# Optimization experiments

Hardware: AMD Instinct MI355X
Metric: run time of the kernel (lower is better)

## Reference

```python
import jax, jax.numpy as jnp
import numpy as np

B, C, H, W = 8, 128, 64, 64
GROUPS = 8
EPS = 1e-5


def setup_inputs() -> dict:
    key = jax.random.key(0)
    ks = jax.random.split(key, 4)
    x = jax.random.normal(ks[0], (B, C, H, W), dtype=jnp.float32)
    gamma = jnp.ones((C,), jnp.float32)
    beta = jnp.zeros((C,), jnp.float32)
    w_qkv = jax.random.normal(ks[1], (3 * C, C), jnp.float32) * (C ** -0.5)
    b_qkv = jnp.zeros((3 * C,), jnp.float32)
    w_proj = jax.random.normal(ks[2], (C, C), jnp.float32) * (C ** -0.5)
    b_proj = jnp.zeros((C,), jnp.float32)
    return {"x": x, "gamma": gamma, "beta": beta, "w_qkv": w_qkv,
            "b_qkv": b_qkv, "w_proj": w_proj, "b_proj": b_proj}


def group_norm(x, gamma, beta):
    b, c, h, w = x.shape
    xg = x.reshape(b, GROUPS, c // GROUPS, h, w)
    mean = xg.mean(axis=(2, 3, 4), keepdims=True)
    var = xg.var(axis=(2, 3, 4), keepdims=True)
    xn = ((xg - mean) * jax.lax.rsqrt(var + EPS)).reshape(b, c, h, w)
    return xn * gamma[None, :, None, None] + beta[None, :, None, None]


def reference(x, gamma, beta, w_qkv, b_qkv, w_proj, b_proj):
    b, c, h, w = x.shape
    n = h * w
    hn = group_norm(x, gamma, beta)
    # 1x1 conv == channel matmul
    qkv = jnp.einsum('oc,bchw->bohw', w_qkv, hn) + b_qkv[None, :, None, None]
    q, k, v = jnp.split(qkv.reshape(b, 3 * c, n), 3, axis=1)  # each [b,c,n]
    attn = jax.nn.softmax(jnp.einsum('bci,bcj->bij', q, k) * (c ** -0.5), axis=-1)
    out = jnp.einsum('bij,bcj->bci', attn, v).reshape(b, c, h, w)
    proj = jnp.einsum('oc,bchw->bohw', w_proj, out) + b_proj[None, :, None, None]
    return x + proj
```

## Files before the change

### kernel.cpp

```cpp
#include <hip/hip_runtime.h>
#include <cstdint>

#define NB 8
#define NC 128
#define NPIX 4096
#define NGROUP 8
#define CPG 16
#define EPS_GN 1e-5f
#define QSCALE 0.12751879523604132f
#define NSPLIT 2
#define JTILES (NPIX / 64 / NSPLIT)

typedef __attribute__((ext_vector_type(8))) short short8;
typedef __attribute__((ext_vector_type(16))) float f32x16;

typedef __attribute__((address_space(1))) const void gvoid_t;
typedef __attribute__((address_space(3))) void svoid_t;

__device__ __forceinline__ unsigned packbf(float lo, float hi) {
  unsigned r;
  asm("v_cvt_pk_bf16_f32 %0, %1, %2" : "=v"(r) : "v"(lo), "v"(hi));
  return r;
}
__device__ __forceinline__ ushort bf16of(float v) {
  return (ushort)(packbf(v, v) & 0xffffu);
}
__device__ __forceinline__ float bfl(unsigned w) {
  return __builtin_bit_cast(float, w << 16);
}
__device__ __forceinline__ float bfh(unsigned w) {
  return __builtin_bit_cast(float, w & 0xffff0000u);
}

__device__ __forceinline__ int swK(int row) {
  return ((row & 7) << 1) | ((row >> 3) & 1);
}

__global__ __launch_bounds__(256) void k_wprep(const float* __restrict__ wqkv,
                                               const float* __restrict__ wproj,
                                               ushort* __restrict__ wbuf) {
  int gi = blockIdx.x * 256 + threadIdx.x;
  int t = gi >> 11, ci = gi & 2047;
  int o = ci >> 4, cc = (ci & 15) ^ (o & 7);
  const float* src = (t < 3) ? (wqkv + ((size_t)(t * 128 + o) * 128 + cc * 8))
                             : (wproj + ((size_t)o * 128 + cc * 8));
  float4 a = *(const float4*)src;
  float4 b2 = *(const float4*)(src + 4);
  uint4 pk;
  pk.x = packbf(a.x, a.y);  pk.y = packbf(a.z, a.w);
  pk.z = packbf(b2.x, b2.y); pk.w = packbf(b2.z, b2.w);
  *(uint4*)&wbuf[(size_t)gi << 3] = pk;
}

__global__ __launch_bounds__(256) void k_gn_stats(const float* __restrict__ x,
                                                  float* __restrict__ stats) {
  int blk = blockIdx.x;
  const float4* base = (const float4*)(x + (size_t)blk * CPG * NPIX);
  float s = 0.f, ss = 0.f;
  for (int i = threadIdx.x; i < CPG * NPIX / 4; i += 256) {
    float4 v = base[i];
    s  += v.x + v.y + v.z + v.w;
    ss += v.x * v.x + v.y * v.y + v.z * v.z + v.w * v.w;
  }
#pragma unroll
  for (int off = 32; off >= 1; off >>= 1) {
    s  += __shfl_down(s, off);
    ss += __shfl_down(ss, off);
  }
  __shared__ float red[8];
  int wid = threadIdx.x >> 6;
  if ((threadIdx.x & 63) == 0) { red[wid] = s; red[4 + wid] = ss; }
  __syncthreads();
  if (threadIdx.x == 0) {
    float S  = red[0] + red[1] + red[2] + red[3];
    float SS = red[4] + red[5] + red[6] + red[7];
    float mean = S * (1.f / (CPG * NPIX));
    float var  = SS * (1.f / (CPG * NPIX)) - mean * mean;
    stats[blk * 2]     = mean;
    stats[blk * 2 + 1] = rsqrtf(var + EPS_GN);
  }
}

__global__ __launch_bounds__(256) void k_qkv(const float* __restrict__ x,
                                             const float* __restrict__ stats,
                                             const float* __restrict__ gamma,
                                             const float* __restrict__ beta,
                                             const ushort* __restrict__ wbuf,
                                             const float* __restrict__ bias,
                                             ushort* __restrict__ qT,
                                             ushort* __restrict__ kT,
                                             ushort* __restrict__ vB) {
  __shared__ ushort At[128 * 128];
  __shared__ ushort Bt[128 * 128];
  __shared__ float sArr[128], tArr[128], biasS[384];
  int b = blockIdx.x, pt = blockIdx.y;
  int p0 = pt * 128;
  int tid = threadIdx.x;
  if (tid < 128) {
    int g = tid >> 4;
    float mean = stats[(b * NGROUP + g) * 2];
    float rstd = stats[(b * NGROUP + g) * 2 + 1];
    float sc = rstd * gamma[tid];
    sArr[tid] = sc;
    tArr[tid] = beta[tid] - mean * sc;
  }
  for (int i = tid; i < 384; i += 256) biasS[i] = bias[i];
  __syncthreads();
  const float* xb = x + (size_t)b * NC * NPIX;
#pragma unroll
  for (int u = 0; u < 8; ++u) {
    int task = tid + u * 256;
    int p = task & 127, cc = task >> 7;
    int c0 = cc * 8;
    float v[8];
#pragma unroll
    for (int i = 0; i < 8; ++i)
      v[i] = sArr[c0 + i] * xb[(size_t)(c0 + i) * NPIX + p0 + p] + tArr[c0 + i];
    uint4 pk;
    pk.x = packbf(v[0], v[1]); pk.y = packbf(v[2], v[3]);
    pk.z = packbf(v[4], v[5]); pk.w = packbf(v[6], v[7]);
    *(uint4*)&Bt[((p << 4) + (cc ^ (p & 7))) << 3] = pk;
  }
  int lane = tid & 63, wv = tid >> 6;
  int lq = lane & 31, h = lane >> 5;

  for (int ot = 0; ot < 3; ++ot) {
    __syncthreads();
#pragma unroll
    for (int u = 0; u < 8; ++u) {
      int g = u * 4 + wv;
      __builtin_amdgcn_global_load_lds(
          (gvoid_t*)(wbuf + (((size_t)ot * 2048 + g * 64 + lane) << 3)),
          (svoid_t*)(At + (g << 9)), 16, 0, 0);
    }
    __syncthreads();
    short8 af[8];
    int arow = wv * 32 + lq;
#pragma unroll
    for (int kk = 0; kk < 8; ++kk) {
      int ch = kk * 2 + h;
      af[kk] = *(const short8*)&At[((arow << 4) + (ch ^ (arow & 7))) << 3];
    }
#pragma unroll
    for (int np = 0; np < 2; ++np) {
      int nt0 = np * 2, nt1 = np * 2 + 1;
      int br0 = nt0 * 32 + lq, br1 = nt1 * 32 + lq;
      f32x16 a0, a1;
#pragma unroll
      for (int r = 0; r < 16; ++r) { a0[r] = 0.f; a1[r] = 0.f; }
      __builtin_amdgcn_s_setprio(1);
#pragma unroll
      for (int kk = 0; kk < 8; ++kk) {
        int ch = kk * 2 + h;
        short8 h0 = *(const short8*)&Bt[((br0 << 4) + (ch ^ (br0 & 7))) << 3];
        short8 h1 = *(const short8*)&Bt[((br1 << 4) + (ch ^ (br1 & 7))) << 3];
        a0 = __builtin_amdgcn_mfma_f32_32x32x16_bf16(af[kk], h0, a0, 0, 0, 0);
        a1 = __builtin_amdgcn_mfma_f32_32x32x16_bf16(af[kk], h1, a1, 0, 0, 0);
      }
      __builtin_amdgcn_s_setprio(0);
#pragma unroll
      for (int half = 0; half < 2; ++half) {
        f32x16& acc = half ? a1 : a0;
        int pg = p0 + (half ? nt1 : nt0) * 32 + lq;
        if (ot < 2) {
          ushort* dst = (ot == 0) ? qT : kT;
          float sc = (ot == 0) ? QSCALE : 1.0f;
#pragma unroll
          for (int g2 = 0; g2 < 4; ++g2) {
            int orow = wv * 32 + 4 * h + 8 * g2;
            uint2 st;
            st.x = packbf((acc[g2 * 4 + 0] + biasS[ot * 128 + orow + 0]) * sc,
                          (acc[g2 * 4 + 1] + biasS[ot * 128 + orow + 1]) * sc);
            st.y = packbf((acc[g2 * 4 + 2] + biasS[ot * 128 + orow + 2]) * sc,
                          (acc[g2 * 4 + 3] + biasS[ot * 128 + orow + 3]) * sc);
            *(uint2*)&dst[(((size_t)b << 12) + pg) * 128 + orow] = st;
          }
        } else {
#pragma unroll
          for (int r = 0; r < 16; ++r) {
            int orow = wv * 32 + (r & 3) + 8 * (r >> 2) + 4 * h;
            float vv = acc[r] + biasS[256 + orow];
            vB[((size_t)(b * 128 + orow) << 12) + pg] = bf16of(vv);
          }
        }
      }
    }
  }
}

__device__ __forceinline__ void attn_tile(const ushort* __restrict__ cur,
                                          const short8 (&qf)[8],
                                          f32x16 (&pacc)[4],
                                          float& m_run, float& l_run,
                                          int lq, int h, int swk) {
  f32x16 s0, s1;
#pragma unroll
  for (int r = 0; r < 16; ++r) { s0[r] = 0.f; s1[r] = 0.f; }
  __builtin_amdgcn_s_setprio(1);
#pragma unroll
  for (int kk = 0; kk < 8; ++kk) {
    int ch = (kk << 1) + h;
    short8 kf0 = *(const short8*)&cur[(((lq) << 4) + (ch ^ swk)) << 3];
    short8 kf1 = *(const short8*)&cur[(((32 + lq) << 4) + (ch ^ swk)) << 3];
    s0 = __builtin_amdgcn_mfma_f32_32x32x16_bf16(kf0, qf[kk], s0, 0, 0, 0);
    s1 = __builtin_amdgcn_mfma_f32_32x32x16_bf16(kf1, qf[kk], s1, 0, 0, 0);
  }
  __builtin_amdgcn_s_setprio(0);

  float tm[8];
#pragma unroll
  for (int r = 0; r < 8; ++r)
    tm[r] = fmaxf(fmaxf(s0[2 * r], s0[2 * r + 1]), fmaxf(s1[2 * r], s1[2 * r + 1]));
  float tmax = fmaxf(fmaxf(fmaxf(tm[0], tm[1]), fmaxf(tm[2], tm[3])),
                     fmaxf(fmaxf(tm[4], tm[5]), fmaxf(tm[6], tm[7])));
  tmax = fmaxf(tmax, __shfl_xor(tmax, 32));

  bool noresc = __all(tmax - m_run <= 8.f);
  float mcur = noresc ? m_run : fmaxf(m_run, tmax);

#pragma unroll
  for (int r = 0; r < 16; ++r) { s0[r] = exp2f(s0[r] - mcur); }
#pragma unroll
  for (int r = 0; r < 16; ++r) { s1[r] = exp2f(s1[r] - mcur); }
  float a0 = (s0[0] + s0[1]) + (s0[2] + s0[3]);
  float a1 = (s0[4] + s0[5]) + (s0[6] + s0[7]);
  float a2 = (s0[8] + s0[9]) + (s0[10] + s0[11]);
  float a3 = (s0[12] + s0[13]) + (s0[14] + s0[15]);
  float a4 = (s1[0] + s1[1]) + (s1[2] + s1[3]);
  float a5 = (s1[4] + s1[5]) + (s1[6] + s1[7]);
  float a6 = (s1[8] + s1[9]) + (s1[10] + s1[11]);
  float a7 = (s1[12] + s1[13]) + (s1[14] + s1[15]);
  float sum = ((a0 + a1) + (a2 + a3)) + ((a4 + a5) + (a6 + a7));
  sum += __shfl_xor(sum, 32);

  if (noresc) {
    l_run += sum;
  } else {
    float alpha = exp2f(m_run - mcur);
    m_run = mcur;
    l_run = l_run * alpha + sum;
#pragma unroll
    for (int r = 0; r < 16; ++r) {
      int qr = (r & 3) + ((r >> 2) << 3) + (h << 2);
      float av = __shfl(alpha, qr);
      pacc[0][r] *= av; pacc[1][r] *= av; pacc[2][r] *= av; pacc[3][r] *= av;
    }
  }

  short8 pa[4];
#pragma unroll
  for (int kk = 0; kk < 4; ++kk) {
    float v0, v1, v2, v3, v4, v5, v6, v7;
    if (kk == 0)      { v0=s0[0];v1=s0[1];v2=s0[2];v3=s0[3];v4=s0[4];v5=s0[5];v6=s0[6];v7=s0[7]; }
    else if (kk == 1) { v0=s0[8];v1=s0[9];v2=s0[10];v3=s0[11];v4=s0[12];v5=s0[13];v6=s0[14];v7=s0[15]; }
    else if (kk == 2) { v0=s1[0];v1=s1[1];v2=s1[2];v3=s1[3];v4=s1[4];v5=s1[5];v6=s1[6];v7=s1[7]; }
    else              { v0=s1[8];v1=s1[9];v2=s1[10];v3=s1[11];v4=s1[12];v5=s1[13];v6=s1[14];v7=s1[15]; }
    unsigned P0a = packbf(v0, v1), P0b = packbf(v2, v3);
    unsigned P1a = packbf(v4, v5), P1b = packbf(v6, v7);
    unsigned sA = h ? P0a : P1a, sB = h ? P0b : P1b;
    unsigned rA = (unsigned)__shfl_xor((int)sA, 32);
    unsigned rB = (unsigned)__shfl_xor((int)sB, 32);
    uint4 wv;
    wv.x = h ? rA : P0a;  wv.y = h ? rB : P0b;
    wv.z = h ? P1a : rA;  wv.w = h ? P1b : rB;
    pa[kk] = __builtin_bit_cast(short8, wv);
  }

  __builtin_amdgcn_s_setprio(1);
#pragma unroll
  for (int nt = 0; nt < 4; ++nt) {
    int row = (nt << 5) + lq;
#pragma unroll
    for (int kk = 0; kk < 4; ++kk) {
      int ch = (kk << 1) + h;
      short8 vf = *(const short8*)&cur[8192 + (((row << 3) + (ch ^ (lq & 7))) << 3)];
      pacc[nt] = __builtin_amdgcn_mfma_f32_32x32x16_bf16(pa[kk], vf, pacc[nt], 0, 0, 0);
    }
  }
  __builtin_amdgcn_s_setprio(0);
}

__global__ __launch_bounds__(256, 2) void k_attn(const ushort* __restrict__ qT,
                                                 const ushort* __restrict__ kT,
                                                 const ushort* __restrict__ vB,
                                                 ushort* __restrict__ attP,
                                                 float2* __restrict__ mlv) {
  __shared__ ushort lds[32768];
  int tid = threadIdx.x;
  int b = blockIdx.x, qt = blockIdx.y, s = blockIdx.z;
  int wid = tid >> 6;
  int lane = tid & 63;
  int lq = lane & 31;
  int h = lane >> 5;
  int swk = swK(lq);
  int q0 = qt * 128 + wid * 32;
  int jbase = s * (NPIX / NSPLIT);

  short8 qf[8];
  const ushort* qp = qT + (((size_t)b << 12) + q0 + lq) * 128 + h * 8;
#pragma unroll
  for (int kk = 0; kk < 8; ++kk) qf[kk] = *(const short8*)(qp + kk * 16);

  f32x16 pacc[4];
#pragma unroll
  for (int nt = 0; nt < 4; ++nt)
#pragma unroll
    for (int r = 0; r < 16; ++r) pacc[nt][r] = 0.f;
  float m_run = -1e30f, l_run = 0.f;

  int id0 = wid * 64 + lane;
  int krow0 = id0 >> 4, kch0 = id0 & 15;
  int vrow0 = id0 >> 3, vch0 = id0 & 7;
  const ushort* kbase = kT + (((size_t)b << 12) + jbase + krow0) * 128 +
                        ((kch0 ^ swK(krow0)) << 3);
  const ushort* vbase = vB + ((size_t)(b * 128 + vrow0) << 12) + jbase +
                        ((vch0 ^ (vrow0 & 7)) << 3);
  int tstage = 0;

#define STAGE(SEL)                                                              \
  do {                                                                          \
    if (tstage < JTILES) {                                                      \
      ushort* dbase = lds + (SEL) * 16384;                                      \
      _Pragma("unroll") for (int u = 0; u < 4; ++u) {                           \
        __builtin_amdgcn_global_load_lds((gvoid_t*)(kbase + u * 2048),          \
            (svoid_t*)(dbase + (u * 4 + wid) * 512), 16, 0, 0);                 \
        __builtin_amdgcn_global_load_lds((gvoid_t*)(vbase + u * 131072),        \
            (svoid_t*)(dbase + 8192 + (u * 4 + wid) * 512), 16, 0, 0);          \
      }                                                                         \
      kbase += 8192;                                       \
      vbase += 64;                                                 \
      ++tstage;                                                                 \
    }                                                                           \
  } while (0)

  STAGE(0);
  for (int it = 0; it < JTILES / 2; ++it) {
    __syncthreads();
    STAGE(1);
    attn_tile(lds, qf, pacc, m_run, l_run, lq, h, swk);
    __syncthreads();
    STAGE(0);
    attn_tile(lds + 16384, qf, pacc, m_run, l_run, lq, h, swk);
  }
#undef STAGE

  size_t sb = (size_t)(s * NB + b);
#pragma unroll
  for (int r = 0; r < 16; ++r) {
    int qr = (r & 3) + ((r >> 2) << 3) + (h << 2);
    size_t rowbase = (((sb << 12) + q0 + qr) << 7) + lq;
    attP[rowbase]      = bf16of(pacc[0][r]);
    attP[rowbase + 32] = bf16of(pacc[1][r]);
    attP[rowbase + 64] = bf16of(pacc[2][r]);
    attP[rowbase + 96] = bf16of(pacc[3][r]);
  }
  if (h == 0) {
    mlv[(sb << 12) + q0 + lq] = make_float2(m_run, l_run);
  }
}

__global__ __launch_bounds__(256) void k_proj(const float* __restrict__ x,
                                              const ushort* __restrict__ attP,
                                              const float2* __restrict__ mlv,
                                              const ushort* __restrict__ wbuf,
                                              const float* __restrict__ bias,
                                              float* __restrict__ out) {
  __shared__ ushort At[128 * 128];
  __shared__ ushort Bt[128 * 128];
  __shared__ float c0s[128], c1s[128], biasS[128];
  int b = blockIdx.x, pt = blockIdx.y;
  int p0 = pt * 128;
  int tid = threadIdx.x;
  int lane = tid & 63, wv = tid >> 6;
#pragma unroll
  for (int u = 0; u < 8; ++u) {
    int g = u * 4 + wv;
    __builtin_amdgcn_global_load_lds(
        (gvoid_t*)(wbuf + (((size_t)3 * 2048 + g * 64 + lane) << 3)),
        (svoid_t*)(At + (g << 9)), 16, 0, 0);
  }
  if (tid < 128) {
    float2 ml0 = mlv[(((size_t)b) << 12) + p0 + tid];
    float2 ml1 = mlv[(((size_t)(NB + b)) << 12) + p0 + tid];
    float M = fmaxf(ml0.x, ml1.x);
    float e0 = exp2f(ml0.x - M), e1 = exp2f(ml1.x - M);
    float inv = 1.f / (ml0.y * e0 + ml1.y * e1);
    c0s[tid] = e0 * inv;
    c1s[tid] = e1 * inv;
    biasS[tid] = bias[tid];
  }
  __syncthreads();
#pragma unroll
  for (int u = 0; u < 8; ++u) {
    int task = tid + u * 256;
    int p = task & 127, cc = task >> 7;
    const ushort* a0p = attP + ((((size_t)b << 12) + p0 + p) << 7) + cc * 8;
    const ushort* a1p = attP + ((((size_t)(NB + b) << 12) + p0 + p) << 7) + cc * 8;
    uint4 u0 = *(const uint4*)a0p;
    uint4 u1 = *(const uint4*)a1p;
    float c0 = c0s[p], c1 = c1s[p];
    uint4 pk;
    pk.x = packbf(bfl(u0.x) * c0 + bfl(u1.x) * c1,
                  bfh(u0.x) * c0 + bfh(u1.x) * c1);
    pk.y = packbf(bfl(u0.y) * c0 + bfl(u1.y) * c1,
                  bfh(u0.y) * c0 + bfh(u1.y) * c1);
    pk.z = packbf(bfl(u0.z) * c0 + bfl(u1.z) * c1,
                  bfh(u0.z) * c0 + bfh(u1.z) * c1);
    pk.w = packbf(bfl(u0.w) * c0 + bfl(u1.w) * c1,
                  bfh(u0.w) * c0 + bfh(u1.w) * c1);
    *(uint4*)&Bt[((p << 4) + (cc ^ (p & 7))) << 3] = pk;
  }
  __syncthreads();
  int lq = lane & 31, h = lane >> 5;
  short8 af[8];
  int arow = wv * 32 + lq;
#pragma unroll
  for (int kk = 0; kk < 8; ++kk) {
    int ch = kk * 2 + h;
    af[kk] = *(const short8*)&At[((arow << 4) + (ch ^ (arow & 7))) << 3];
  }
  const float* xb = x + (size_t)b * NC * NPIX;
  float* ob = out + (size_t)b * NC * NPIX;
#pragma unroll
  for (int np = 0; np < 2; ++np) {
    int nt0 = np * 2, nt1 = np * 2 + 1;
    int br0 = nt0 * 32 + lq, br1 = nt1 * 32 + lq;
    f32x16 a0, a1;
#pragma unroll
    for (int r = 0; r < 16; ++r) { a0[r] = 0.f; a1[r] = 0.f; }
    __builtin_amdgcn_s_setprio(1);
#pragma unroll
    for (int kk = 0; kk < 8; ++kk) {
      int ch = kk * 2 + h;
      short8 h0 = *(const short8*)&Bt[((br0 << 4) + (ch ^ (br0 & 7))) << 3];
      short8 h1 = *(const short8*)&Bt[((br1 << 4) + (ch ^ (br1 & 7))) << 3];
      a0 = __builtin_amdgcn_mfma_f32_32x32x16_bf16(af[kk], h0, a0, 0, 0, 0);
      a1 = __builtin_amdgcn_mfma_f32_32x32x16_bf16(af[kk], h1, a1, 0, 0, 0);
    }
    __builtin_amdgcn_s_setprio(0);
#pragma unroll
    for (int half = 0; half < 2; ++half) {
      f32x16& acc = half ? a1 : a0;
      int pg = p0 + (half ? nt1 : nt0) * 32 + lq;
#pragma unroll
      for (int r = 0; r < 16; ++r) {
        int orow = wv * 32 + (r & 3) + 8 * (r >> 2) + 4 * h;
        size_t idx = ((size_t)orow << 12) + pg;
        ob[idx] = acc[r] + biasS[orow] + xb[idx];
      }
    }
  }
}

extern "C" void kernel_launch(void* const* d_in, const int* in_sizes, int n_in,
                              void* d_out, int out_size, void* d_ws, size_t ws_size,
                              hipStream_t stream) {
  const float* x      = (const float*)d_in[0];
  const float* gamma  = (const float*)d_in[1];
  const float* beta   = (const float*)d_in[2];
  const float* w_qkv  = (const float*)d_in[3];
  const float* b_qkv  = (const float*)d_in[4];
  const float* w_proj = (const float*)d_in[5];
  const float* b_proj = (const float*)d_in[6];
  float* out = (float*)d_out;
  char* wsb = (char*)d_ws;

  float*  stats = (float*)wsb;
  ushort* qT    = (ushort*)(wsb + 1024);
  ushort* kT    = (ushort*)(wsb + 1024 + (8u << 20));
  ushort* vB    = (ushort*)(wsb + 1024 + (16u << 20));
  ushort* attP  = (ushort*)(wsb + 1024 + (24u << 20));
  float2* mlv   = (float2*)(wsb + 1024 + (40u << 20));
  ushort* wbuf  = (ushort*)(wsb + 1024 + (41u << 20));

  hipLaunchKernelGGL(k_wprep, dim3(32), dim3(256), 0, stream, w_qkv, w_proj, wbuf);
  hipLaunchKernelGGL(k_gn_stats, dim3(NB * NGROUP), dim3(256), 0, stream, x, stats);
  hipLaunchKernelGGL(k_qkv, dim3(NB, NPIX / 128), dim3(256), 0, stream,
                     x, stats, gamma, beta, wbuf, b_qkv, qT, kT, vB);
  hipLaunchKernelGGL(k_attn, dim3(NB, NPIX / 128, NSPLIT), dim3(256), 0, stream,
                     qT, kT, vB, attP, mlv);
  hipLaunchKernelGGL(k_proj, dim3(NB, NPIX / 128), dim3(256), 0, stream,
                     x, attP, mlv, wbuf, b_proj, out);
}
```

Before: 144.3 us.

## Merge weight prep and GN stats kernels; split QK accumulators; defer row-sum

Merges the weight bf16 conversion and group-norm statistics kernels into one launch that picks its role by block index, removing one kernel launch. In the attention tile, the QK^T MFMA chain is split into two independent accumulator pairs and summed at the end, shortening the dependent MFMA chain. The softmax row-sum reduction is moved after the PV MFMAs so it can overlap with them. The extra accumulators raise register pressure, which matters under the 2-block occupancy bound.

Result: faster. 139.0 us (-3.7%).

```diff
diff --git a/kernel.cpp b/kernel.cpp
--- a/kernel.cpp
+++ b/kernel.cpp
@@ -36,48 +36,49 @@
   return ((row & 7) << 1) | ((row >> 3) & 1);
 }
 
-__global__ __launch_bounds__(256) void k_wprep(const float* __restrict__ wqkv,
-                                               const float* __restrict__ wproj,
-                                               ushort* __restrict__ wbuf) {
-  int gi = blockIdx.x * 256 + threadIdx.x;
-  int t = gi >> 11, ci = gi & 2047;
-  int o = ci >> 4, cc = (ci & 15) ^ (o & 7);
-  const float* src = (t < 3) ? (wqkv + ((size_t)(t * 128 + o) * 128 + cc * 8))
-                             : (wproj + ((size_t)o * 128 + cc * 8));
-  float4 a = *(const float4*)src;
-  float4 b2 = *(const float4*)(src + 4);
-  uint4 pk;
-  pk.x = packbf(a.x, a.y);  pk.y = packbf(a.z, a.w);
-  pk.z = packbf(b2.x, b2.y); pk.w = packbf(b2.z, b2.w);
-  *(uint4*)&wbuf[(size_t)gi << 3] = pk;
-}
-
-__global__ __launch_bounds__(256) void k_gn_stats(const float* __restrict__ x,
-                                                  float* __restrict__ stats) {
+__global__ __launch_bounds__(256) void k_pre(const float* __restrict__ x,
+                                             float* __restrict__ stats,
+                                             const float* __restrict__ wqkv,
+                                             const float* __restrict__ wproj,
+                                             ushort* __restrict__ wbuf) {
   int blk = blockIdx.x;
-  const float4* base = (const float4*)(x + (size_t)blk * CPG * NPIX);
-  float s = 0.f, ss = 0.f;
-  for (int i = threadIdx.x; i < CPG * NPIX / 4; i += 256) {
-    float4 v = base[i];
-    s  += v.x + v.y + v.z + v.w;
-    ss += v.x * v.x + v.y * v.y + v.z * v.z + v.w * v.w;
-  }
-#pragma unroll
-  for (int off = 32; off >= 1; off >>= 1) {
-    s  += __shfl_down(s, off);
-    ss += __shfl_down(ss, off);
-  }
-  __shared__ float red[8];
-  int wid = threadIdx.x >> 6;
-  if ((threadIdx.x & 63) == 0) { red[wid] = s; red[4 + wid] = ss; }
-  __syncthreads();
-  if (threadIdx.x == 0) {
-    float S  = red[0] + red[1] + red[2] + red[3];
-    float SS = red[4] + red[5] + red[6] + red[7];
-    float mean = S * (1.f / (CPG * NPIX));
-    float var  = SS * (1.f / (CPG * NPIX)) - mean * mean;
-    stats[blk * 2]     = mean;
-    stats[blk * 2 + 1] = rsqrtf(var + EPS_GN);
+  if (blk < 64) {
+    const float4* base = (const float4*)(x + (size_t)blk * CPG * NPIX);
+    float s = 0.f, ss = 0.f;
+    for (int i = threadIdx.x; i < CPG * NPIX / 4; i += 256) {
+      float4 v = base[i];
+      s  += v.x + v.y + v.z + v.w;
+      ss += v.x * v.x + v.y * v.y + v.z * v.z + v.w * v.w;
+    }
+#pragma unroll
+    for (int off = 32; off >= 1; off >>= 1) {
+      s  += __shfl_down(s, off);
+      ss += __shfl_down(ss, off);
+    }
+    __shared__ float red[8];
+    int wid = threadIdx.x >> 6;
+    if ((threadIdx.x & 63) == 0) { red[wid] = s; red[4 + wid] = ss; }
+    __syncthreads();
+    if (threadIdx.x == 0) {
+      float S  = red[0] + red[1] + red[2] + red[3];
+      float SS = red[4] + red[5] + red[6] + red[7];
+      float mean = S * (1.f / (CPG * NPIX));
+      float var  = SS * (1.f / (CPG * NPIX)) - mean * mean;
+      stats[blk * 2]     = mean;
+      stats[blk * 2 + 1] = rsqrtf(var + EPS_GN);
+    }
+  } else {
+    int gi = (blk - 64) * 256 + threadIdx.x;
+    int t = gi >> 11, ci = gi & 2047;
+    int o = ci >> 4, cc = (ci & 15) ^ (o & 7);
+    const float* src = (t < 3) ? (wqkv + ((size_t)(t * 128 + o) * 128 + cc * 8))
+                               : (wproj + ((size_t)o * 128 + cc * 8));
+    float4 a = *(const float4*)src;
+    float4 b2 = *(const float4*)(src + 4);
+    uint4 pk;
+    pk.x = packbf(a.x, a.y);  pk.y = packbf(a.z, a.w);
+    pk.z = packbf(b2.x, b2.y); pk.w = packbf(b2.z, b2.w);
+    *(uint4*)&wbuf[(size_t)gi << 3] = pk;
   }
 }
 
@@ -193,19 +194,26 @@
                                           f32x16 (&pacc)[4],
                                           float& m_run, float& l_run,
                                           int lq, int h, int swk) {
-  f32x16 s0, s1;
-#pragma unroll
-  for (int r = 0; r < 16; ++r) { s0[r] = 0.f; s1[r] = 0.f; }
+  f32x16 s0, s1, s0b, s1b;
+#pragma unroll
+  for (int r = 0; r < 16; ++r) { s0[r] = 0.f; s1[r] = 0.f; s0b[r] = 0.f; s1b[r] = 0.f; }
   __builtin_amdgcn_s_setprio(1);
 #pragma unroll
-  for (int kk = 0; kk < 8; ++kk) {
-    int ch = (kk << 1) + h;
-    short8 kf0 = *(const short8*)&cur[(((lq) << 4) + (ch ^ swk)) << 3];
-    short8 kf1 = *(const short8*)&cur[(((32 + lq) << 4) + (ch ^ swk)) << 3];
-    s0 = __builtin_amdgcn_mfma_f32_32x32x16_bf16(kf0, qf[kk], s0, 0, 0, 0);
-    s1 = __builtin_amdgcn_mfma_f32_32x32x16_bf16(kf1, qf[kk], s1, 0, 0, 0);
+  for (int kp = 0; kp < 4; ++kp) {
+    int chA = (kp << 2) + h;
+    int chB = (kp << 2) + 2 + h;
+    short8 k0A = *(const short8*)&cur[(((lq) << 4) + (chA ^ swk)) << 3];
+    short8 k1A = *(const short8*)&cur[(((32 + lq) << 4) + (chA ^ swk)) << 3];
+    short8 k0B = *(const short8*)&cur[(((lq) << 4) + (chB ^ swk)) << 3];
+    short8 k1B = *(const short8*)&cur[(((32 + lq) << 4) + (chB ^ swk)) << 3];
+    s0  = __builtin_amdgcn_mfma_f32_32x32x16_bf16(k0A, qf[2 * kp],     s0,  0, 0, 0);
+    s1  = __builtin_amdgcn_mfma_f32_32x32x16_bf16(k1A, qf[2 * kp],     s1,  0, 0, 0);
+    s0b = __builtin_amdgcn_mfma_f32_32x32x16_bf16(k0B, qf[2 * kp + 1], s0b, 0, 0, 0);
+    s1b = __builtin_amdgcn_mfma_f32_32x32x16_bf16(k1B, qf[2 * kp + 1], s1b, 0, 0, 0);
   }
   __builtin_amdgcn_s_setprio(0);
+#pragma unroll
+  for (int r = 0; r < 16; ++r) { s0[r] += s0b[r]; s1[r] += s1b[r]; }
 
   float tm[8];
 #pragma unroll
@@ -222,23 +230,11 @@
   for (int r = 0; r < 16; ++r) { s0[r] = exp2f(s0[r] - mcur); }
 #pragma unroll
   for (int r = 0; r < 16; ++r) { s1[r] = exp2f(s1[r] - mcur); }
-  float a0 = (s0[0] + s0[1]) + (s0[2] + s0[3]);
-  float a1 = (s0[4] + s0[5]) + (s0[6] + s0[7]);
-  float a2 = (s0[8] + s0[9]) + (s0[10] + s0[11]);
-  float a3 = (s0[12] + s0[13]) + (s0[14] + s0[15]);
-  float a4 = (s1[0] + s1[1]) + (s1[2] + s1[3]);
-  float a5 = (s1[4] + s1[5]) + (s1[6] + s1[7]);
-  float a6 = (s1[8] + s1[9]) + (s1[10] + s1[11]);
-  float a7 = (s1[12] + s1[13]) + (s1[14] + s1[15]);
-  float sum = ((a0 + a1) + (a2 + a3)) + ((a4 + a5) + (a6 + a7));
-  sum += __shfl_xor(sum, 32);
-
-  if (noresc) {
-    l_run += sum;
-  } else {
-    float alpha = exp2f(m_run - mcur);
+
+  float alpha = 1.f;
+  if (!noresc) {
+    alpha = exp2f(m_run - mcur);
     m_run = mcur;
-    l_run = l_run * alpha + sum;
 #pragma unroll
     for (int r = 0; r < 16; ++r) {
       int qr = (r & 3) + ((r >> 2) << 3) + (h << 2);
@@ -278,6 +274,18 @@
     }
   }
   __builtin_amdgcn_s_setprio(0);
+
+  float a0 = (s0[0] + s0[1]) + (s0[2] + s0[3]);
+  float a1 = (s0[4] + s0[5]) + (s0[6] + s0[7]);
+  float a2 = (s0[8] + s0[9]) + (s0[10] + s0[11]);
+  float a3 = (s0[12] + s0[13]) + (s0[14] + s0[15]);
+  float a4 = (s1[0] + s1[1]) + (s1[2] + s1[3]);
+  float a5 = (s1[4] + s1[5]) + (s1[6] + s1[7]);
+  float a6 = (s1[8] + s1[9]) + (s1[10] + s1[11]);
+  float a7 = (s1[12] + s1[13]) + (s1[14] + s1[15]);
+  float sum = ((a0 + a1) + (a2 + a3)) + ((a4 + a5) + (a6 + a7));
+  sum += __shfl_xor(sum, 32);
+  l_run = noresc ? (l_run + sum) : (l_run * alpha + sum);
 }
 
 __global__ __launch_bounds__(256, 2) void k_attn(const ushort* __restrict__ qT,
@@ -473,8 +481,8 @@
   float2* mlv   = (float2*)(wsb + 1024 + (40u << 20));
   ushort* wbuf  = (ushort*)(wsb + 1024 + (41u << 20));
 
-  hipLaunchKernelGGL(k_wprep, dim3(32), dim3(256), 0, stream, w_qkv, w_proj, wbuf);
-  hipLaunchKernelGGL(k_gn_stats, dim3(NB * NGROUP), dim3(256), 0, stream, x, stats);
+  hipLaunchKernelGGL(k_pre, dim3(96), dim3(256), 0, stream,
+                     x, stats, w_qkv, w_proj, wbuf);
   hipLaunchKernelGGL(k_qkv, dim3(NB, NPIX / 128), dim3(256), 0, stream,
                      x, stats, gamma, beta, wbuf, b_qkv, qT, kT, vB);
   hipLaunchKernelGGL(k_attn, dim3(NB, NPIX / 128, NSPLIT), dim3(256), 0, stream,
```
